# Optimization experiments

Measured on AMD Instinct MI355X. Metric: run time of the kernel, lower is better.

## Reference

```python
import jax, jax.numpy as jnp
import numpy as np

N_NODES = 50000
N_EDGES = 800000
IN_CH = 256
OUT_CH = 64  # heads=1
NEG_SLOPE = 0.2


def setup_inputs() -> dict:
    key = jax.random.key(0)
    k1, k2, k3, k4, k5 = jax.random.split(key, 5)
    x = jax.random.normal(k1, (N_NODES, IN_CH), dtype=jnp.float32)
    edge_index = jax.random.randint(k2, (2, N_EDGES), 0, N_NODES, dtype=jnp.int64)
    # glorot init for dense weight [out, in] (torch Linear layout) and att [out, 2]
    s_w = np.sqrt(6.0 / (OUT_CH + IN_CH)).astype(np.float32)
    W = jax.random.uniform(k3, (OUT_CH, IN_CH), minval=-s_w, maxval=s_w, dtype=jnp.float32)
    b = jnp.zeros((OUT_CH,), dtype=jnp.float32)
    s_a = np.sqrt(6.0 / (OUT_CH + 2)).astype(np.float32)
    att = jax.random.uniform(k4, (OUT_CH, 2), minval=-s_a, maxval=s_a, dtype=jnp.float32)
    return {"x": x, "edge_index": edge_index, "W": W, "b": b, "att": att}


def reference(x, edge_index, W, b, att):
    n = x.shape[0]
    # dense projection: feature [N, OUT_CH]
    feature = x @ W.T + b
    # per-node attention contributions: e_pre [N, 2]
    e_pre = feature @ att
    tar = edge_index[0]  # flow='target_to_source'
    src = edge_index[1]
    # edge logit = leakyrelu(a_tar(t) + a_src(s)); self-loop logit per node
    logit_edge = jax.nn.leaky_relu(e_pre[tar, 0] + e_pre[src, 1], NEG_SLOPE)
    logit_self = jax.nn.leaky_relu(e_pre[:, 0] + e_pre[:, 1], NEG_SLOPE)
    # segment softmax over {self edge} U {incoming edges} per target node
    m = jnp.maximum(jax.ops.segment_max(logit_edge, tar, num_segments=n), logit_self)
    exp_edge = jnp.exp(logit_edge - m[tar])
    exp_self = jnp.exp(logit_self - m)
    denom = exp_self + jax.ops.segment_sum(exp_edge, tar, num_segments=n)
    alpha = exp_edge / denom[tar]          # [E]
    alpha_self = exp_self / denom          # [N]
    # weighted gather-scatter aggregation (fused_gas_agg)
    msgs = alpha[:, None] * feature[src]   # [E, OUT_CH]
    out = alpha_self[:, None] * feature + jax.ops.segment_sum(msgs, tar, num_segments=n)
    return out
```

## Files before the change

### kernel.cpp

```cpp
#include <hip/hip_runtime.h>
#include <math.h>

#define N_NODES 50000
#define N_EDGES 800000
#define IN_CH 256
#define OUT_CH 64
#define NEG_SLOPE 0.2f
#define PAD 64
#define DEGS 16

typedef __bf16 bf16x4 __attribute__((ext_vector_type(4)));
typedef __bf16 bf16x8 __attribute__((ext_vector_type(8)));
typedef float  f32x4  __attribute__((ext_vector_type(4)));

__global__ __launch_bounds__(256) void k_gemm(
    const float* __restrict__ x, const float* __restrict__ W,
    const float* __restrict__ bias, const float* __restrict__ att,
    __bf16* __restrict__ featb, float* __restrict__ e0,
    float* __restrict__ e1, int* __restrict__ deg)
{
    __shared__ __bf16 B[64][264];

    const int t    = threadIdx.x;
    const int row0 = blockIdx.x * 64;
    const int wv   = t >> 6;
    const int li   = t & 63;
    const int lm   = li & 15;
    const int lq   = li >> 4;

    {
        int idx = row0 * DEGS + t * 4;
        if (idx + 3 < N_NODES * DEGS)
            *reinterpret_cast<int4*>(&deg[idx]) = make_int4(0, 0, 0, 0);
        else {
            #pragma unroll
            for (int j = 0; j < 4; ++j)
                if (idx + j < N_NODES * DEGS) deg[idx + j] = 0;
        }
    }

    {
        const int sr = t >> 2;
        const int cq = t & 3;
        #pragma unroll
        for (int j = 0; j < 4; ++j) {
            #pragma unroll
            for (int i = 0; i < 4; ++i) {
                int kk = j * 64 + cq * 16 + i * 4;
                float4 w1 = *reinterpret_cast<const float4*>(&W[(size_t)sr * IN_CH + kk]);
                bf16x4 g = {(__bf16)w1.x, (__bf16)w1.y, (__bf16)w1.z, (__bf16)w1.w};
                *reinterpret_cast<bf16x4*>(&B[sr][kk]) = g;
            }
        }
    }
    __syncthreads();

    const int myrow = row0 + wv * 16 + lm;
    const float* xrow = x + (size_t)(myrow < N_NODES ? myrow : 0) * IN_CH;

    f32x4 acc[4];
    #pragma unroll
    for (int tn = 0; tn < 4; ++tn) acc[tn] = (f32x4){0.f, 0.f, 0.f, 0.f};

    #pragma unroll
    for (int kb = 0; kb < 8; ++kb) {
        int ko = kb * 32 + lq * 8;
        float4 a0 = *reinterpret_cast<const float4*>(&xrow[ko]);
        float4 a1 = *reinterpret_cast<const float4*>(&xrow[ko + 4]);
        bf16x8 a = {(__bf16)a0.x, (__bf16)a0.y, (__bf16)a0.z, (__bf16)a0.w,
                    (__bf16)a1.x, (__bf16)a1.y, (__bf16)a1.z, (__bf16)a1.w};
        #pragma unroll
        for (int tn = 0; tn < 4; ++tn) {
            bf16x8 b = *reinterpret_cast<const bf16x8*>(&B[tn * 16 + lm][ko]);
            acc[tn] = __builtin_amdgcn_mfma_f32_16x16x32_bf16(a, b, acc[tn], 0, 0, 0);
        }
    }

    float att0[4], att1[4], bv[4];
    #pragma unroll
    for (int tn = 0; tn < 4; ++tn) {
        int c = tn * 16 + lm;
        att0[tn] = att[c * 2 + 0];
        att1[tn] = att[c * 2 + 1];
        bv[tn]   = bias[c];
    }

    float p0[4] = {0.f, 0.f, 0.f, 0.f};
    float p1[4] = {0.f, 0.f, 0.f, 0.f};
    #pragma unroll
    for (int r = 0; r < 4; ++r) {
        int row = row0 + wv * 16 + lq * 4 + r;
        #pragma unroll
        for (int tn = 0; tn < 4; ++tn) {
            float f = acc[tn][r] + bv[tn];
            if (row < N_NODES)
                featb[(size_t)row * OUT_CH + tn * 16 + lm] = (__bf16)f;
            p0[r] += f * att0[tn];
            p1[r] += f * att1[tn];
        }
    }

    #pragma unroll
    for (int m = 1; m < 16; m <<= 1) {
        #pragma unroll
        for (int r = 0; r < 4; ++r) {
            p0[r] += __shfl_xor(p0[r], m, 64);
            p1[r] += __shfl_xor(p1[r], m, 64);
        }
    }
    if (lm == 0) {
        #pragma unroll
        for (int r = 0; r < 4; ++r) {
            int row = row0 + wv * 16 + lq * 4 + r;
            if (row < N_NODES) {
                e0[row] = p0[r];
                e1[row] = p1[r];
            }
        }
    }
}

__global__ __launch_bounds__(256) void k_build(
    const int* __restrict__ ei, int* __restrict__ deg,
    unsigned short* __restrict__ pcsr)
{
    int e = blockIdx.x * blockDim.x + threadIdx.x;
    if (e >= N_EDGES) return;
    int tnode = ei[e];
    int snode = ei[N_EDGES + e];
    int slot = atomicAdd(&deg[tnode * DEGS], 1);
    if (slot < PAD)
        pcsr[(size_t)tnode * PAD + slot] = (unsigned short)snode;
}

__global__ __launch_bounds__(256) void k_gather(
    const float* __restrict__ e0, const float* __restrict__ e1,
    const __bf16* __restrict__ featb, const int* __restrict__ deg,
    const unsigned short* __restrict__ pcsr, float* __restrict__ out)
{
    int t    = blockIdx.x * 4 + (threadIdx.x >> 6);
    int lane = threadIdx.x & 63;
    if (t >= N_NODES) return;

    int cnt = deg[t * DEGS];
    cnt = cnt > PAD ? PAD : cnt;

    float e0t = e0[t];

    int si = (int)pcsr[(size_t)t * PAD + lane];
    si = (lane < cnt) ? si : 0;
    float qi = e1[si];
    float zi = e0t + qi;
    float wi = (lane < cnt) ? __expf(zi > 0.f ? zi : NEG_SLOPE * zi) : 0.f;

    float zs  = e0t + e1[t];
    float wsf = __expf(zs > 0.f ? zs : NEG_SLOPE * zs);

    float wsum = wi;
    #pragma unroll
    for (int m = 1; m < 64; m <<= 1)
        wsum += __shfl_xor(wsum, m, 64);
    wsum += wsf;

    float acc = wsf * (float)featb[(size_t)t * OUT_CH + lane];

    int i = 0;
    for (; i + 4 <= cnt; i += 4) {
        int   s0 = __builtin_amdgcn_readlane(si, i);
        int   s1 = __builtin_amdgcn_readlane(si, i + 1);
        int   s2 = __builtin_amdgcn_readlane(si, i + 2);
        int   s3 = __builtin_amdgcn_readlane(si, i + 3);
        float w0 = __uint_as_float(__builtin_amdgcn_readlane(__float_as_uint(wi), i));
        float w1 = __uint_as_float(__builtin_amdgcn_readlane(__float_as_uint(wi), i + 1));
        float w2 = __uint_as_float(__builtin_amdgcn_readlane(__float_as_uint(wi), i + 2));
        float w3 = __uint_as_float(__builtin_amdgcn_readlane(__float_as_uint(wi), i + 3));
        float f0 = (float)featb[(size_t)s0 * OUT_CH + lane];
        float f1 = (float)featb[(size_t)s1 * OUT_CH + lane];
        float f2 = (float)featb[(size_t)s2 * OUT_CH + lane];
        float f3 = (float)featb[(size_t)s3 * OUT_CH + lane];
        acc += w0 * f0 + w1 * f1 + w2 * f2 + w3 * f3;
    }
    for (; i < cnt; ++i) {
        int   s0 = __builtin_amdgcn_readlane(si, i);
        float w0 = __uint_as_float(__builtin_amdgcn_readlane(__float_as_uint(wi), i));
        acc += w0 * (float)featb[(size_t)s0 * OUT_CH + lane];
    }

    out[(size_t)t * OUT_CH + lane] = acc / wsum;
}

extern "C" void kernel_launch(void* const* d_in, const int* in_sizes, int n_in,
                              void* d_out, int out_size, void* d_ws, size_t ws_size,
                              hipStream_t stream)
{
    const float* x    = (const float*)d_in[0];
    const int*   ei   = (const int*)d_in[1];
    const float* W    = (const float*)d_in[2];
    const float* bias = (const float*)d_in[3];
    const float* att  = (const float*)d_in[4];
    float* out = (float*)d_out;

    __bf16* featb = (__bf16*)d_ws;
    float*  e0    = (float*)(featb + (size_t)N_NODES * OUT_CH);
    float*  e1    = e0 + N_NODES;
    int*    deg   = (int*)(e1 + N_NODES);
    unsigned short* pcsr = (unsigned short*)(deg + (size_t)N_NODES * DEGS);

    dim3 blk(256);

    k_gemm<<<dim3((N_NODES + 63) / 64), blk, 0, stream>>>(
        x, W, bias, att, featb, e0, e1, deg);

    k_build<<<dim3((N_EDGES + 255) / 256), blk, 0, stream>>>(ei, deg, pcsr);

    k_gather<<<dim3((N_NODES + 3) / 4), blk, 0, stream>>>(
        e0, e1, featb, deg, pcsr, out);
}
```

Baseline: 174.5 us.

## Fuse CSR build into GEMM kernel so edge atomics overlap the projection

Merges the edge-bucketing pass into the GEMM launch. The first block range processes 16 edges per thread with vectorized index loads and atomics, and the remaining blocks run the bf16 MFMA projection, so the atomic-bound build can overlap the compute-bound GEMM. Degree zeroing moves into a separate small kernel that runs first, because the fused blocks need deg cleared before any atomics. This adds one launch and a harder-to-tune block partition, and in return removes a serialized launch and its tail.

```diff
diff --git a/kernel.cpp b/kernel.cpp
--- a/kernel.cpp
+++ b/kernel.cpp
@@ -9,35 +9,67 @@
 #define PAD 64
 #define DEGS 16
 
+#define EDGE_BLOCKS 196
+#define GEMM_BLOCKS 782
+
 typedef __bf16 bf16x4 __attribute__((ext_vector_type(4)));
 typedef __bf16 bf16x8 __attribute__((ext_vector_type(8)));
 typedef float  f32x4  __attribute__((ext_vector_type(4)));
 
-__global__ __launch_bounds__(256) void k_gemm(
+__global__ __launch_bounds__(256) void k_zero(int* __restrict__ deg)
+{
+    int idx = (blockIdx.x * 256 + threadIdx.x) * 4;
+    if (idx + 4 <= N_NODES * DEGS)
+        *reinterpret_cast<int4*>(&deg[idx]) = make_int4(0, 0, 0, 0);
+}
+
+__global__ __launch_bounds__(256) void k_fused(
     const float* __restrict__ x, const float* __restrict__ W,
     const float* __restrict__ bias, const float* __restrict__ att,
+    const int* __restrict__ ei,
     __bf16* __restrict__ featb, float* __restrict__ e0,
-    float* __restrict__ e1, int* __restrict__ deg)
+    float* __restrict__ e1, int* __restrict__ deg,
+    unsigned short* __restrict__ pcsr)
 {
     __shared__ __bf16 B[64][264];
 
-    const int t    = threadIdx.x;
-    const int row0 = blockIdx.x * 64;
+    const int t = threadIdx.x;
+
+    if (blockIdx.x < EDGE_BLOCKS) {
+        const int base = blockIdx.x * 4096 + t * 4;
+        int tn[16], sn[16], sl[16];
+        #pragma unroll
+        for (int c = 0; c < 4; ++c) {
+            int e = base + c * 1024;
+            if (e + 4 <= N_EDGES) {
+                *reinterpret_cast<int4*>(&tn[c * 4]) =
+                    *reinterpret_cast<const int4*>(&ei[e]);
+                *reinterpret_cast<int4*>(&sn[c * 4]) =
+                    *reinterpret_cast<const int4*>(&ei[N_EDGES + e]);
+            } else {
+                #pragma unroll
+                for (int j = 0; j < 4; ++j) {
+                    int ee = e + j;
+                    tn[c * 4 + j] = (ee < N_EDGES) ? ei[ee] : -1;
+                    sn[c * 4 + j] = (ee < N_EDGES) ? ei[N_EDGES + ee] : 0;
+                }
+            }
+        }
+        #pragma unroll
+        for (int k = 0; k < 16; ++k)
+            sl[k] = (tn[k] >= 0) ? atomicAdd(&deg[tn[k] * DEGS], 1) : 0x7fffffff;
+        #pragma unroll
+        for (int k = 0; k < 16; ++k)
+            if (tn[k] >= 0 && sl[k] < PAD)
+                pcsr[(size_t)tn[k] * PAD + sl[k]] = (unsigned short)sn[k];
+        return;
+    }
+
+    const int row0 = (blockIdx.x - EDGE_BLOCKS) * 64;
     const int wv   = t >> 6;
     const int li   = t & 63;
     const int lm   = li & 15;
     const int lq   = li >> 4;
-
-    {
-        int idx = row0 * DEGS + t * 4;
-        if (idx + 3 < N_NODES * DEGS)
-            *reinterpret_cast<int4*>(&deg[idx]) = make_int4(0, 0, 0, 0);
-        else {
-            #pragma unroll
-            for (int j = 0; j < 4; ++j)
-                if (idx + j < N_NODES * DEGS) deg[idx + j] = 0;
-        }
-    }
 
     {
         const int sr = t >> 2;
@@ -118,19 +150,6 @@
             }
         }
     }
-}
-
-__global__ __launch_bounds__(256) void k_build(
-    const int* __restrict__ ei, int* __restrict__ deg,
-    unsigned short* __restrict__ pcsr)
-{
-    int e = blockIdx.x * blockDim.x + threadIdx.x;
-    if (e >= N_EDGES) return;
-    int tnode = ei[e];
-    int snode = ei[N_EDGES + e];
-    int slot = atomicAdd(&deg[tnode * DEGS], 1);
-    if (slot < PAD)
-        pcsr[(size_t)tnode * PAD + slot] = (unsigned short)snode;
 }
 
 __global__ __launch_bounds__(256) void k_gather(
@@ -208,10 +227,10 @@
 
     dim3 blk(256);
 
-    k_gemm<<<dim3((N_NODES + 63) / 64), blk, 0, stream>>>(
-        x, W, bias, att, featb, e0, e1, deg);
-
-    k_build<<<dim3((N_EDGES + 255) / 256), blk, 0, stream>>>(ei, deg, pcsr);
+    k_zero<<<dim3((N_NODES * DEGS / 4 + 255) / 256), blk, 0, stream>>>(deg);
+
+    k_fused<<<dim3(EDGE_BLOCKS + GEMM_BLOCKS), blk, 0, stream>>>(
+        x, W, bias, att, ei, featb, e0, e1, deg, pcsr);
 
     k_gather<<<dim3((N_NODES + 3) / 4), blk, 0, stream>>>(
         e0, e1, featb, deg, pcsr, out);
```

Result: faster. 166.8 us (-4.4%).
